# Kernel tuning notes

Hardware: AMD Instinct MI355X
Metric: run time of the kernel (lower is better)

## Reference

```python
import jax, jax.numpy as jnp
import numpy as np

B, S, D_IN, UNITS = 8, 2048, 512, 512


def _glorot(key, fan_in, fan_out):
    limit = np.sqrt(6.0 / (fan_in + fan_out)).astype(np.float32)
    return jax.random.uniform(key, (fan_in, fan_out), jnp.float32, -limit, limit)


def setup_inputs() -> dict:
    key = jax.random.key(0)
    kq, kwq, kwv, kwk = jax.random.split(key, 4)
    return {
        "query": jax.random.normal(kq, (B, S, D_IN), jnp.float32),
        "Wq": _glorot(kwq, D_IN, UNITS),   # W_query conv1d k=1, no bias
        "Wv": _glorot(kwv, D_IN, UNITS),   # W_value conv1d k=1, no bias
        "Wk": _glorot(kwk, D_IN, UNITS),   # W_key   conv1d k=1, no bias
    }


def reference(query, Wq, Wv, Wk):
    # Pointwise causal Conv1D(kernel=1, no bias) with sigmoid activation == sigmoid(x @ W)
    q = jax.nn.sigmoid(jnp.einsum('bsd,du->bsu', query, Wq))   # W_query(query)
    k = jax.nn.sigmoid(jnp.einsum('bsd,du->bsu', query, Wv))   # W_value(key=query)
    v = jax.nn.sigmoid(jnp.einsum('bsd,du->bsu', query, Wk))   # W_key(value=query)

    d_in = query.shape[-1]  # scaling uses value's input feature dim, not units
    score = jnp.einsum('bqu,bku->bqk', q, k) / jnp.sqrt(jnp.float32(d_in))  # [B,S,S]

    # Mask: upper triangle INCLUDING diagonal is -inf (strictly-causal, no self)
    s = score.shape[1]
    masked = jnp.where(jnp.triu(jnp.ones((s, s), bool)), -jnp.inf, score)

    # Row 0 is fully masked -> replaced by zeros; rows 1: softmax over j < i
    rest = jax.nn.softmax(masked[:, 1:, :], axis=-1)
    attn = jnp.concatenate([jnp.zeros((score.shape[0], 1, s), score.dtype), rest], axis=1)

    return jnp.einsum('bqk,bku->bqu', attn, v)
```

## Files before the change

### kernel.cpp

```cpp
#include <hip/hip_runtime.h>
#include <stdint.h>


typedef __attribute__((ext_vector_type(4))) float f32x4;
typedef __attribute__((ext_vector_type(8))) short short8;
typedef __attribute__((ext_vector_type(4))) short short4b;

__device__ __forceinline__ short f2bf(float f) {
    union { float f; uint32_t u; } v; v.f = f;
    uint32_t r = (v.u + 0x7FFFu + ((v.u >> 16) & 1u)) >> 16;
    return (short)r;
}
__device__ __forceinline__ float bf2f(short s) {
    union { uint32_t u; float f; } v; v.u = ((uint32_t)(uint16_t)s) << 16; return v.f;
}
__device__ __forceinline__ float sigm(float x) { return 1.0f / (1.0f + __expf(-x)); }

__device__ __forceinline__ void gload_lds16(const void* g, void* l) {
    __builtin_amdgcn_global_load_lds(
        (const __attribute__((address_space(1))) void*)g,
        (__attribute__((address_space(3))) void*)l, 16, 0, 0);
}

__global__ __launch_bounds__(256) void fused_prep(
    const float* __restrict__ X, const float* __restrict__ Wq,
    const float* __restrict__ Wv, const float* __restrict__ Wk,
    short* __restrict__ Xb, short* __restrict__ Wt)
{
    __shared__ float T[64 * 68];
    if (blockIdx.x < 4096) {
        size_t i = (size_t)blockIdx.x * 256 + threadIdx.x;
        const float4* src = reinterpret_cast<const float4*>(X) + i * 2;
        float4 a = src[0], b = src[1];
        short8 o;
        o[0] = f2bf(a.x); o[1] = f2bf(a.y); o[2] = f2bf(a.z); o[3] = f2bf(a.w);
        o[4] = f2bf(b.x); o[5] = f2bf(b.y); o[6] = f2bf(b.z); o[7] = f2bf(b.w);
        *reinterpret_cast<short8*>(Xb + i * 8) = o;
        return;
    }
    int bid = blockIdx.x - 4096;
    int w = bid >> 6;
    int tile = bid & 63;
    int n0 = (tile & 7) * 64;
    int k0 = (tile >> 3) * 64;
    const float* W = (w == 0) ? Wq : (w == 1) ? Wv : Wk;
    int t = threadIdx.x;
    int tr = t >> 4, tc = t & 15;
    for (int rr = 0; rr < 4; ++rr) {
        int row = rr * 16 + tr;
        float4 v = *reinterpret_cast<const float4*>(&W[(size_t)(k0 + row) * 512 + n0 + tc * 4]);
        T[row * 68 + tc * 4 + 0] = v.x;
        T[row * 68 + tc * 4 + 1] = v.y;
        T[row * 68 + tc * 4 + 2] = v.z;
        T[row * 68 + tc * 4 + 3] = v.w;
    }
    __syncthreads();
    for (int wr = 0; wr < 4; ++wr) {
        int nl = wr * 16 + tr;
        short4b o;
        for (int i = 0; i < 4; ++i) o[i] = f2bf(T[(tc * 4 + i) * 68 + nl]);
        *reinterpret_cast<short4b*>(&Wt[((size_t)(w * 512 + n0 + nl)) * 512 + k0 + tc * 4]) = o;
    }
}

__global__ __launch_bounds__(256) void qkv_gemm(
    const short* __restrict__ Xb,
    const short* __restrict__ Wt,
    short* __restrict__ Qb, short* __restrict__ Kb, short* __restrict__ VtG)
{
    __shared__ short SMEM[128 * 128];
    short* As = SMEM;
    short* Bs = SMEM + 128 * 64;

    int bx = blockIdx.x;
    int mt = bx & 127;
    int y = bx >> 7;
    int w = y >> 2, nt = y & 3;
    int m0 = mt * 128, n0 = nt * 128;

    int tid = threadIdx.x;
    int wv = tid >> 6, lane = tid & 63;
    int wr = wv >> 1, wc = wv & 1;
    int ln = lane & 15, hi = lane >> 4;

    f32x4 acc[4][4];
#pragma unroll
    for (int i = 0; i < 4; ++i)
#pragma unroll
        for (int j = 0; j < 4; ++j) acc[i][j] = {0.f, 0.f, 0.f, 0.f};

    const short* Asrc = Xb + (size_t)m0 * 512;
    const short* Bsrc = Wt + (size_t)w * 512 * 512 + (size_t)n0 * 512;

    for (int ko = 0; ko < 8; ++ko) {
        int k0 = ko * 64;
#pragma unroll
        for (int j = 0; j < 4; ++j) {
            int r = wv * 8 + j * 32 + (lane >> 3);
            int sc = ((lane & 7) * 8) ^ ((r & 7) << 3);
            gload_lds16(Asrc + (size_t)r * 512 + k0 + sc, &As[(wv * 8 + j * 32) * 64]);
        }
#pragma unroll
        for (int j = 0; j < 4; ++j) {
            int r = wv * 8 + j * 32 + (lane >> 3);
            int sc = ((lane & 7) * 8) ^ ((r & 7) << 3);
            gload_lds16(Bsrc + (size_t)r * 512 + k0 + sc, &Bs[(wv * 8 + j * 32) * 64]);
        }
        __syncthreads();
#pragma unroll
        for (int kk = 0; kk < 2; ++kk) {
            int kof = kk * 32 + hi * 8;
            int sw = (ln & 7) << 3;
            short8 af[4], bf[4];
#pragma unroll
            for (int mf = 0; mf < 4; ++mf)
                af[mf] = *reinterpret_cast<const short8*>(&As[(wr * 64 + mf * 16 + ln) * 64 + (kof ^ sw)]);
#pragma unroll
            for (int nf = 0; nf < 4; ++nf)
                bf[nf] = *reinterpret_cast<const short8*>(&Bs[(wc * 64 + nf * 16 + ln) * 64 + (kof ^ sw)]);
#pragma unroll
            for (int mf = 0; mf < 4; ++mf)
#pragma unroll
                for (int nf = 0; nf < 4; ++nf)
                    acc[mf][nf] = __builtin_amdgcn_mfma_f32_16x16x32_bf16(af[mf], bf[nf], acc[mf][nf], 0, 0, 0);
        }
        __syncthreads();
    }

    if (w < 2) {
        short* O = (w == 0) ? Qb : Kb;
#pragma unroll
        for (int mf = 0; mf < 4; ++mf)
#pragma unroll
            for (int nf = 0; nf < 4; ++nf)
#pragma unroll
                for (int j = 0; j < 4; ++j) {
                    int row = m0 + wr * 64 + mf * 16 + hi * 4 + j;
                    int col = n0 + wc * 64 + nf * 16 + ln;
                    O[(size_t)row * 512 + col] = f2bf(sigm(acc[mf][nf][j]));
                }
    } else {
#pragma unroll
        for (int mf = 0; mf < 4; ++mf)
#pragma unroll
            for (int nf = 0; nf < 4; ++nf)
#pragma unroll
                for (int j = 0; j < 4; ++j) {
                    int ml = wr * 64 + mf * 16 + hi * 4 + j;
                    int nl = wc * 64 + nf * 16 + ln;
                    SMEM[nl * 128 + (ml ^ ((nl & 7) << 3))] = f2bf(sigm(acc[mf][nf][j]));
                }
        __syncthreads();
        int bb = m0 >> 11;
        int s0 = m0 & 2047;
        int d = tid >> 1, h = tid & 1;
#pragma unroll
        for (int i = 0; i < 8; ++i) {
            int s8 = h * 64 + i * 8;
            short8 v = *reinterpret_cast<const short8*>(&SMEM[d * 128 + (s8 ^ ((d & 7) << 3))]);
            *reinterpret_cast<short8*>(&VtG[((size_t)(bb * 512 + n0 + d)) * 2048 + s0 + s8]) = v;
        }
    }
}

__global__ __launch_bounds__(256) void score_pass(
    const short* __restrict__ Qb, const short* __restrict__ Kb,
    short* __restrict__ Pc, float* __restrict__ Dpart)
{
    __shared__ short SMEM[128 * 128];
    __shared__ float psum[2][128];
    short* As = SMEM;
    short* Bs = SMEM + 128 * 64;

    const float scale = 0.044194173824159216f;

    int bid = blockIdx.x;
    int b = bid & 7;
    int idx = bid >> 3;
    int ti = 0;
    while ((ti + 1) * (ti + 2) / 2 <= idx) ++ti;
    int tj = idx - ti * (ti + 1) / 2;
    int m0 = ti * 128, n0 = tj * 128;

    int tid = threadIdx.x;
    int w = tid >> 6, lane = tid & 63;
    int wr = w >> 1, wc = w & 1;
    int ln = lane & 15, hi = lane >> 4;

    const short* Qsrc = Qb + (size_t)b * 2048 * 512 + (size_t)m0 * 512;
    const short* Ksrc = Kb + (size_t)b * 2048 * 512 + (size_t)n0 * 512;

    f32x4 acc[4][4];
#pragma unroll
    for (int i = 0; i < 4; ++i)
#pragma unroll
        for (int j = 0; j < 4; ++j) acc[i][j] = {0.f, 0.f, 0.f, 0.f};

    for (int ko = 0; ko < 8; ++ko) {
        int k0 = ko * 64;
#pragma unroll
        for (int j = 0; j < 4; ++j) {
            int r = w * 8 + j * 32 + (lane >> 3);
            int sc = ((lane & 7) * 8) ^ ((r & 7) << 3);
            gload_lds16(Qsrc + (size_t)r * 512 + k0 + sc, &As[(w * 8 + j * 32) * 64]);
        }
#pragma unroll
        for (int j = 0; j < 4; ++j) {
            int r = w * 8 + j * 32 + (lane >> 3);
            int sc = ((lane & 7) * 8) ^ ((r & 7) << 3);
            gload_lds16(Ksrc + (size_t)r * 512 + k0 + sc, &Bs[(w * 8 + j * 32) * 64]);
        }
        __syncthreads();
#pragma unroll
        for (int kk = 0; kk < 2; ++kk) {
            int kof = kk * 32 + hi * 8;
            int sw = (ln & 7) << 3;
            short8 af[4], bf[4];
#pragma unroll
            for (int mf = 0; mf < 4; ++mf)
                af[mf] = *reinterpret_cast<const short8*>(&As[(wr * 64 + mf * 16 + ln) * 64 + (kof ^ sw)]);
#pragma unroll
            for (int nf = 0; nf < 4; ++nf)
                bf[nf] = *reinterpret_cast<const short8*>(&Bs[(wc * 64 + nf * 16 + ln) * 64 + (kof ^ sw)]);
#pragma unroll
            for (int mf = 0; mf < 4; ++mf)
#pragma unroll
                for (int nf = 0; nf < 4; ++nf)
                    acc[mf][nf] = __builtin_amdgcn_mfma_f32_16x16x32_bf16(af[mf], bf[nf], acc[mf][nf], 0, 0, 0);
        }
        __syncthreads();
    }

    short* Ptile = Pc + (size_t)(b * 136 + idx) * 128 * 128;
#pragma unroll
    for (int mf = 0; mf < 4; ++mf) {
        float rs[4] = {0.f, 0.f, 0.f, 0.f};
#pragma unroll
        for (int nf = 0; nf < 4; ++nf)
#pragma unroll
            for (int j = 0; j < 4; ++j) {
                int rl = wr * 64 + mf * 16 + hi * 4 + j;
                int cl = wc * 64 + nf * 16 + ln;
                int irow = m0 + rl, jcol = n0 + cl;
                float p = (jcol < irow) ? __expf(acc[mf][nf][j] * scale) : 0.f;
                short hs = f2bf(p);
                Ptile[(size_t)rl * 128 + cl] = hs;
                rs[j] += bf2f(hs);
            }
#pragma unroll
        for (int j = 0; j < 4; ++j) {
            float s = rs[j];
            s += __shfl_xor(s, 1);
            s += __shfl_xor(s, 2);
            s += __shfl_xor(s, 4);
            s += __shfl_xor(s, 8);
            if (ln == 0) psum[wc][wr * 64 + mf * 16 + hi * 4 + j] = s;
        }
    }
    __syncthreads();
    if (tid < 128)
        Dpart[((size_t)b * 16 + tj) * 2048 + m0 + tid] = psum[0][tid] + psum[1][tid];
}

__global__ __launch_bounds__(256) void pv_pass(
    const short* __restrict__ Pc, const short* __restrict__ VtG,
    const float* __restrict__ Dpart, float* __restrict__ Out)
{
    __shared__ short SMEM[128 * 64 + 64 * 64];
    __shared__ float dnm[128];
    short* As = SMEM;
    short* Bs = SMEM + 128 * 64;

    int bid = blockIdx.x;
    int b = bid & 7;
    int rr = bid >> 3;
    int grp = rr >> 5, off = rr & 31;
    int ti = (grp & 1) ? (15 - (off >> 1)) : (off >> 1);
    int colhalf = 2 * grp + (off & 1);
    int m0 = ti * 128, n0 = colhalf * 64;

    int tid = threadIdx.x;
    int w = tid >> 6, lane = tid & 63;
    int wr = w >> 1, wc = w & 1;
    int ln = lane & 15, hi = lane >> 4;

    if (tid < 128) {
        float s = 0.f;
        for (int tj = 0; tj <= ti; ++tj)
            s += Dpart[((size_t)b * 16 + tj) * 2048 + m0 + tid];
        int gi = m0 + tid;
        dnm[tid] = (gi == 0) ? 0.f : 1.0f / s;
    }

    const short* Ptiles = Pc + (size_t)(b * 136 + ti * (ti + 1) / 2) * 128 * 128;
    const short* Vsrc = VtG + (size_t)b * 512 * 2048 + (size_t)n0 * 2048;

    f32x4 acc[4][2];
#pragma unroll
    for (int i = 0; i < 4; ++i)
#pragma unroll
        for (int j = 0; j < 2; ++j) acc[i][j] = {0.f, 0.f, 0.f, 0.f};

    for (int ks = 0; ks < 2 * (ti + 1); ++ks) {
        int tj = ks >> 1;
        int j0 = (ks & 1) * 64;
        const short* Pt = Ptiles + (size_t)tj * 128 * 128;
#pragma unroll
        for (int j = 0; j < 4; ++j) {
            int r = w * 8 + j * 32 + (lane >> 3);
            int sc = ((lane & 7) * 8) ^ ((r & 7) << 3);
            gload_lds16(Pt + (size_t)r * 128 + j0 + sc, &As[(w * 8 + j * 32) * 64]);
        }
#pragma unroll
        for (int j = 0; j < 2; ++j) {
            int r = w * 8 + j * 32 + (lane >> 3);
            int sc = ((lane & 7) * 8) ^ ((r & 7) << 3);
            gload_lds16(Vsrc + (size_t)r * 2048 + tj * 128 + j0 + sc, &Bs[(w * 8 + j * 32) * 64]);
        }
        __syncthreads();
#pragma unroll
        for (int kk = 0; kk < 2; ++kk) {
            int kof = kk * 32 + hi * 8;
            int sw = (ln & 7) << 3;
            short8 af[4], bf[2];
#pragma unroll
            for (int mf = 0; mf < 4; ++mf)
                af[mf] = *reinterpret_cast<const short8*>(&As[(wr * 64 + mf * 16 + ln) * 64 + (kof ^ sw)]);
#pragma unroll
            for (int nf = 0; nf < 2; ++nf)
                bf[nf] = *reinterpret_cast<const short8*>(&Bs[(wc * 32 + nf * 16 + ln) * 64 + (kof ^ sw)]);
#pragma unroll
            for (int mf = 0; mf < 4; ++mf)
#pragma unroll
                for (int nf = 0; nf < 2; ++nf)
                    acc[mf][nf] = __builtin_amdgcn_mfma_f32_16x16x32_bf16(af[mf], bf[nf], acc[mf][nf], 0, 0, 0);
        }
        __syncthreads();
    }

#pragma unroll
    for (int mf = 0; mf < 4; ++mf)
#pragma unroll
        for (int j = 0; j < 4; ++j) {
            int rl = wr * 64 + mf * 16 + hi * 4 + j;
            float rd = dnm[rl];
            float* orow = Out + ((size_t)b * 2048 + m0 + rl) * 512 + n0 + wc * 32 + ln;
#pragma unroll
            for (int nf = 0; nf < 2; ++nf)
                orow[nf * 16] = acc[mf][nf][j] * rd;
        }
}

extern "C" void kernel_launch(void* const* d_in, const int* in_sizes, int n_in,
                              void* d_out, int out_size, void* d_ws, size_t ws_size,
                              hipStream_t stream) {
    const float* X  = (const float*)d_in[0];
    const float* Wq = (const float*)d_in[1];
    const float* Wv = (const float*)d_in[2];
    const float* Wk = (const float*)d_in[3];
    float* Out = (float*)d_out;

    char* ws = (char*)d_ws;
    const size_t WT_BYTES  = (size_t)3 * 512 * 512 * 2;
    const size_t MAT_BYTES = (size_t)16384 * 512 * 2;
    const size_t PC_BYTES  = (size_t)8 * 136 * 128 * 128 * 2;
    short* Wt = (short*)ws;
    short* Qb = (short*)(ws + WT_BYTES);
    short* Kb = (short*)(ws + WT_BYTES + MAT_BYTES);
    short* Vt = (short*)(ws + WT_BYTES + 2 * MAT_BYTES);
    short* Pc = (short*)(ws + WT_BYTES + 3 * MAT_BYTES);
    short* Xb = Pc;
    float* Dp = (float*)(ws + WT_BYTES + 3 * MAT_BYTES + PC_BYTES);

    fused_prep<<<4288, 256, 0, stream>>>(X, Wq, Wv, Wk, Xb, Wt);
    qkv_gemm<<<1536, 256, 0, stream>>>(Xb, Wt, Qb, Kb, Vt);
    score_pass<<<1088, 256, 0, stream>>>(Qb, Kb, Pc, Dp);
    pv_pass<<<1024, 256, 0, stream>>>(Pc, Vt, Dp, Out);
}
```

Baseline: 136.4 us.

## Pair causal row tiles per PV block and load GEMM B fragments directly

pv_pass now runs 512-thread blocks that each process a complementary pair of causal row tiles (p and 15-p) over a 128-wide column slice, so every block gets the same amount of work. This also widens the N tile so each P tile load is shared by more output columns, and the launch shrinks to 256 blocks. Separately, qkv_gemm reads the weight fragments straight from global memory into registers instead of staging them through LDS. The trade-offs are fewer, heavier blocks (256 blocks on a GPU with many CUs), more accumulator registers, and uncoalesced-ish global B loads in the GEMM.

Result: slower. 158.8 us (+16.4%).

```diff
diff --git a/kernel.cpp b/kernel.cpp
--- a/kernel.cpp
+++ b/kernel.cpp
@@ -70,7 +70,6 @@
 {
     __shared__ short SMEM[128 * 128];
     short* As = SMEM;
-    short* Bs = SMEM + 128 * 64;
 
     int bx = blockIdx.x;
     int mt = bx & 127;
@@ -91,6 +90,7 @@
 
     const short* Asrc = Xb + (size_t)m0 * 512;
     const short* Bsrc = Wt + (size_t)w * 512 * 512 + (size_t)n0 * 512;
+    const short* Bfrag = Bsrc + (size_t)(wc * 64 + ln) * 512 + hi * 8;
 
     for (int ko = 0; ko < 8; ++ko) {
         int k0 = ko * 64;
@@ -100,29 +100,27 @@
             int sc = ((lane & 7) * 8) ^ ((r & 7) << 3);
             gload_lds16(Asrc + (size_t)r * 512 + k0 + sc, &As[(wv * 8 + j * 32) * 64]);
         }
-#pragma unroll
-        for (int j = 0; j < 4; ++j) {
-            int r = wv * 8 + j * 32 + (lane >> 3);
-            int sc = ((lane & 7) * 8) ^ ((r & 7) << 3);
-            gload_lds16(Bsrc + (size_t)r * 512 + k0 + sc, &Bs[(wv * 8 + j * 32) * 64]);
-        }
+        short8 breg[2][4];
+#pragma unroll
+        for (int kk = 0; kk < 2; ++kk)
+#pragma unroll
+            for (int nf = 0; nf < 4; ++nf)
+                breg[kk][nf] = *reinterpret_cast<const short8*>(
+                    Bfrag + (size_t)(nf * 16) * 512 + k0 + kk * 32);
         __syncthreads();
 #pragma unroll
         for (int kk = 0; kk < 2; ++kk) {
             int kof = kk * 32 + hi * 8;
             int sw = (ln & 7) << 3;
-            short8 af[4], bf[4];
+            short8 af[4];
 #pragma unroll
             for (int mf = 0; mf < 4; ++mf)
                 af[mf] = *reinterpret_cast<const short8*>(&As[(wr * 64 + mf * 16 + ln) * 64 + (kof ^ sw)]);
 #pragma unroll
-            for (int nf = 0; nf < 4; ++nf)
-                bf[nf] = *reinterpret_cast<const short8*>(&Bs[(wc * 64 + nf * 16 + ln) * 64 + (kof ^ sw)]);
-#pragma unroll
             for (int mf = 0; mf < 4; ++mf)
 #pragma unroll
                 for (int nf = 0; nf < 4; ++nf)
-                    acc[mf][nf] = __builtin_amdgcn_mfma_f32_16x16x32_bf16(af[mf], bf[nf], acc[mf][nf], 0, 0, 0);
+                    acc[mf][nf] = __builtin_amdgcn_mfma_f32_16x16x32_bf16(af[mf], breg[kk][nf], acc[mf][nf], 0, 0, 0);
         }
         __syncthreads();
     }
@@ -262,93 +260,105 @@
         Dpart[((size_t)b * 16 + tj) * 2048 + m0 + tid] = psum[0][tid] + psum[1][tid];
 }
 
-__global__ __launch_bounds__(256) void pv_pass(
+__global__ __launch_bounds__(512) void pv_pass(
     const short* __restrict__ Pc, const short* __restrict__ VtG,
     const float* __restrict__ Dpart, float* __restrict__ Out)
 {
-    __shared__ short SMEM[128 * 64 + 64 * 64];
-    __shared__ float dnm[128];
-    short* As = SMEM;
-    short* Bs = SMEM + 128 * 64;
+    __shared__ short As[128 * 64];
+    __shared__ short Bs[128 * 64];
+    __shared__ float dnm[2][128];
 
     int bid = blockIdx.x;
     int b = bid & 7;
-    int rr = bid >> 3;
-    int grp = rr >> 5, off = rr & 31;
-    int ti = (grp & 1) ? (15 - (off >> 1)) : (off >> 1);
-    int colhalf = 2 * grp + (off & 1);
-    int m0 = ti * 128, n0 = colhalf * 64;
+    int r5 = bid >> 3;
+    int p = r5 & 7;
+    int dq = r5 >> 3;
+    int n0 = dq * 128;
 
     int tid = threadIdx.x;
-    int w = tid >> 6, lane = tid & 63;
-    int wr = w >> 1, wc = w & 1;
+    int wv = tid >> 6, lane = tid & 63;
+    int wm = wv >> 2, wn = wv & 3;
     int ln = lane & 15, hi = lane >> 4;
 
-    if (tid < 128) {
+    if (tid < 256) {
+        int g = tid >> 7, row = tid & 127;
+        int ti = g ? (15 - p) : p;
         float s = 0.f;
         for (int tj = 0; tj <= ti; ++tj)
-            s += Dpart[((size_t)b * 16 + tj) * 2048 + m0 + tid];
-        int gi = m0 + tid;
-        dnm[tid] = (gi == 0) ? 0.f : 1.0f / s;
-    }
-
-    const short* Ptiles = Pc + (size_t)(b * 136 + ti * (ti + 1) / 2) * 128 * 128;
+            s += Dpart[((size_t)b * 16 + tj) * 2048 + ti * 128 + row];
+        int gi = ti * 128 + row;
+        dnm[g][row] = (gi == 0) ? 0.f : 1.0f / s;
+    }
+
     const short* Vsrc = VtG + (size_t)b * 512 * 2048 + (size_t)n0 * 2048;
 
-    f32x4 acc[4][2];
-#pragma unroll
-    for (int i = 0; i < 4; ++i)
-#pragma unroll
-        for (int j = 0; j < 2; ++j) acc[i][j] = {0.f, 0.f, 0.f, 0.f};
-
-    for (int ks = 0; ks < 2 * (ti + 1); ++ks) {
-        int tj = ks >> 1;
-        int j0 = (ks & 1) * 64;
-        const short* Pt = Ptiles + (size_t)tj * 128 * 128;
-#pragma unroll
-        for (int j = 0; j < 4; ++j) {
-            int r = w * 8 + j * 32 + (lane >> 3);
-            int sc = ((lane & 7) * 8) ^ ((r & 7) << 3);
-            gload_lds16(Pt + (size_t)r * 128 + j0 + sc, &As[(w * 8 + j * 32) * 64]);
-        }
-#pragma unroll
-        for (int j = 0; j < 2; ++j) {
-            int r = w * 8 + j * 32 + (lane >> 3);
-            int sc = ((lane & 7) * 8) ^ ((r & 7) << 3);
-            gload_lds16(Vsrc + (size_t)r * 2048 + tj * 128 + j0 + sc, &Bs[(w * 8 + j * 32) * 64]);
-        }
-        __syncthreads();
-#pragma unroll
-        for (int kk = 0; kk < 2; ++kk) {
-            int kof = kk * 32 + hi * 8;
-            int sw = (ln & 7) << 3;
-            short8 af[4], bf[2];
-#pragma unroll
-            for (int mf = 0; mf < 4; ++mf)
-                af[mf] = *reinterpret_cast<const short8*>(&As[(wr * 64 + mf * 16 + ln) * 64 + (kof ^ sw)]);
-#pragma unroll
-            for (int nf = 0; nf < 2; ++nf)
-                bf[nf] = *reinterpret_cast<const short8*>(&Bs[(wc * 32 + nf * 16 + ln) * 64 + (kof ^ sw)]);
-#pragma unroll
-            for (int mf = 0; mf < 4; ++mf)
+    f32x4 acc[2][4][2];
+#pragma unroll
+    for (int g = 0; g < 2; ++g)
+#pragma unroll
+        for (int i = 0; i < 4; ++i)
+#pragma unroll
+            for (int j = 0; j < 2; ++j) acc[g][i][j] = {0.f, 0.f, 0.f, 0.f};
+
+#pragma unroll
+    for (int g = 0; g < 2; ++g) {
+        int ti = g ? (15 - p) : p;
+        const short* Ptiles = Pc + (size_t)(b * 136 + ti * (ti + 1) / 2) * 16384;
+        for (int ks = 0; ks < 2 * (ti + 1); ++ks) {
+            int tj = ks >> 1;
+            int j0 = (ks & 1) * 64;
+            const short* Pt = Ptiles + (size_t)tj * 16384;
+#pragma unroll
+            for (int j = 0; j < 2; ++j) {
+                int r0 = wv * 16 + j * 8;
+                int r = r0 + (lane >> 3);
+                int sc = ((lane & 7) * 8) ^ ((r & 7) << 3);
+                gload_lds16(Pt + (size_t)r * 128 + j0 + sc, &As[r0 * 64]);
+            }
+#pragma unroll
+            for (int j = 0; j < 2; ++j) {
+                int r0 = wv * 16 + j * 8;
+                int r = r0 + (lane >> 3);
+                int sc = ((lane & 7) * 8) ^ ((r & 7) << 3);
+                gload_lds16(Vsrc + (size_t)r * 2048 + tj * 128 + j0 + sc, &Bs[r0 * 64]);
+            }
+            __syncthreads();
+#pragma unroll
+            for (int kk = 0; kk < 2; ++kk) {
+                int kof = kk * 32 + hi * 8;
+                int sw = (ln & 7) << 3;
+                short8 af[4], bf[2];
+#pragma unroll
+                for (int mf = 0; mf < 4; ++mf)
+                    af[mf] = *reinterpret_cast<const short8*>(&As[(wm * 64 + mf * 16 + ln) * 64 + (kof ^ sw)]);
 #pragma unroll
                 for (int nf = 0; nf < 2; ++nf)
-                    acc[mf][nf] = __builtin_amdgcn_mfma_f32_16x16x32_bf16(af[mf], bf[nf], acc[mf][nf], 0, 0, 0);
-        }
-        __syncthreads();
-    }
-
-#pragma unroll
-    for (int mf = 0; mf < 4; ++mf)
-#pragma unroll
-        for (int j = 0; j < 4; ++j) {
-            int rl = wr * 64 + mf * 16 + hi * 4 + j;
-            float rd = dnm[rl];
-            float* orow = Out + ((size_t)b * 2048 + m0 + rl) * 512 + n0 + wc * 32 + ln;
-#pragma unroll
-            for (int nf = 0; nf < 2; ++nf)
-                orow[nf * 16] = acc[mf][nf][j] * rd;
-        }
+                    bf[nf] = *reinterpret_cast<const short8*>(&Bs[(wn * 32 + nf * 16 + ln) * 64 + (kof ^ sw)]);
+#pragma unroll
+                for (int mf = 0; mf < 4; ++mf)
+#pragma unroll
+                    for (int nf = 0; nf < 2; ++nf)
+                        acc[g][mf][nf] = __builtin_amdgcn_mfma_f32_16x16x32_bf16(af[mf], bf[nf], acc[g][mf][nf], 0, 0, 0);
+            }
+            __syncthreads();
+        }
+    }
+
+#pragma unroll
+    for (int g = 0; g < 2; ++g) {
+        int ti = g ? (15 - p) : p;
+#pragma unroll
+        for (int mf = 0; mf < 4; ++mf)
+#pragma unroll
+            for (int j = 0; j < 4; ++j) {
+                int rl = wm * 64 + mf * 16 + hi * 4 + j;
+                float rd = dnm[g][rl];
+                float* orow = Out + ((size_t)b * 2048 + ti * 128 + rl) * 512 + n0 + wn * 32 + ln;
+#pragma unroll
+                for (int nf = 0; nf < 2; ++nf)
+                    orow[nf * 16] = acc[g][mf][nf][j] * rd;
+            }
+    }
 }
 
 extern "C" void kernel_launch(void* const* d_in, const int* in_sizes, int n_in,
@@ -375,5 +385,5 @@
     fused_prep<<<4288, 256, 0, stream>>>(X, Wq, Wv, Wk, Xb, Wt);
     qkv_gemm<<<1536, 256, 0, stream>>>(Xb, Wt, Qb, Kb, Vt);
     score_pass<<<1088, 256, 0, stream>>>(Qb, Kb, Pc, Dp);
-    pv_pass<<<1024, 256, 0, stream>>>(Pc, Vt, Dp, Out);
-}
+    pv_pass<<<256, 512, 0, stream>>>(Pc, Vt, Dp, Out);
+}
```

## Double-buffer QKV GEMM LDS loads and stage Q/K epilogue through LDS

Applied to the files above, without the earlier changes.

The QKV projection GEMM now keeps two LDS buffers and issues the global-to-LDS loads for the next K step before computing on the current one, using one waitcnt+barrier per iteration instead of two syncthreads. The Q/K epilogue now writes sigmoid outputs into a swizzled LDS tile and stores them with 16-byte vector writes, replacing scattered 2-byte global stores. Launch bounds hint two blocks per CU. LDS use doubles to 64 KB per block, which can limit occupancy. The qkv GEMM is only one of several kernels, so the effect on total time is bounded.

After: 132.7 us, median of 2. -2.7%, faster.

```diff
diff --git a/kernel.cpp b/kernel.cpp
--- a/kernel.cpp
+++ b/kernel.cpp
@@ -21,6 +21,8 @@
         (const __attribute__((address_space(1))) void*)g,
         (__attribute__((address_space(3))) void*)l, 16, 0, 0);
 }
+
+#define VMBAR() asm volatile("s_waitcnt vmcnt(0)\n\ts_barrier" ::: "memory")
 
 __global__ __launch_bounds__(256) void fused_prep(
     const float* __restrict__ X, const float* __restrict__ Wq,
@@ -63,14 +65,12 @@
     }
 }
 
-__global__ __launch_bounds__(256) void qkv_gemm(
+__global__ __launch_bounds__(256, 2) void qkv_gemm(
     const short* __restrict__ Xb,
     const short* __restrict__ Wt,
     short* __restrict__ Qb, short* __restrict__ Kb, short* __restrict__ VtG)
 {
-    __shared__ short SMEM[128 * 128];
-    short* As = SMEM;
-    short* Bs = SMEM + 128 * 64;
+    __shared__ short SMEM[2][16384];
 
     int bx = blockIdx.x;
     int mt = bx & 127;
@@ -92,21 +92,34 @@
     const short* Asrc = Xb + (size_t)m0 * 512;
     const short* Bsrc = Wt + (size_t)w * 512 * 512 + (size_t)n0 * 512;
 
+    int srow = wv * 8 + (lane >> 3);
+    int ssc0 = (lane & 7) * 8;
+
+#define QSTAGE(ko, buf)                                                            \
+    {                                                                              \
+        int _k0 = (ko) * 64;                                                       \
+        _Pragma("unroll")                                                          \
+        for (int _j = 0; _j < 4; ++_j) {                                           \
+            int _r = srow + _j * 32;                                               \
+            int _sc = ssc0 ^ ((_r & 7) << 3);                                      \
+            gload_lds16(Asrc + (size_t)_r * 512 + _k0 + _sc,                       \
+                        &SMEM[buf][(wv * 8 + _j * 32) * 64]);                      \
+        }                                                                          \
+        _Pragma("unroll")                                                          \
+        for (int _j = 0; _j < 4; ++_j) {                                           \
+            int _r = srow + _j * 32;                                               \
+            int _sc = ssc0 ^ ((_r & 7) << 3);                                      \
+            gload_lds16(Bsrc + (size_t)_r * 512 + _k0 + _sc,                       \
+                        &SMEM[buf][8192 + (wv * 8 + _j * 32) * 64]);               \
+        }                                                                          \
+    }
+
+    QSTAGE(0, 0);
     for (int ko = 0; ko < 8; ++ko) {
-        int k0 = ko * 64;
-#pragma unroll
-        for (int j = 0; j < 4; ++j) {
-            int r = wv * 8 + j * 32 + (lane >> 3);
-            int sc = ((lane & 7) * 8) ^ ((r & 7) << 3);
-            gload_lds16(Asrc + (size_t)r * 512 + k0 + sc, &As[(wv * 8 + j * 32) * 64]);
-        }
-#pragma unroll
-        for (int j = 0; j < 4; ++j) {
-            int r = wv * 8 + j * 32 + (lane >> 3);
-            int sc = ((lane & 7) * 8) ^ ((r & 7) << 3);
-            gload_lds16(Bsrc + (size_t)r * 512 + k0 + sc, &Bs[(wv * 8 + j * 32) * 64]);
-        }
-        __syncthreads();
+        VMBAR();
+        if (ko + 1 < 8) QSTAGE(ko + 1, (ko + 1) & 1);
+        const short* As = SMEM[ko & 1];
+        const short* Bs = SMEM[ko & 1] + 8192;
 #pragma unroll
         for (int kk = 0; kk < 2; ++kk) {
             int kof = kk * 32 + hi * 8;
@@ -124,21 +137,31 @@
                 for (int nf = 0; nf < 4; ++nf)
                     acc[mf][nf] = __builtin_amdgcn_mfma_f32_16x16x32_bf16(af[mf], bf[nf], acc[mf][nf], 0, 0, 0);
         }
-        __syncthreads();
-    }
-
+    }
+    __syncthreads();
+#undef QSTAGE
+
+    short* Ts = SMEM[0];
     if (w < 2) {
+#pragma unroll
+        for (int mf = 0; mf < 4; ++mf)
+#pragma unroll
+            for (int nf = 0; nf < 4; ++nf)
+#pragma unroll
+                for (int j = 0; j < 4; ++j) {
+                    int rl = wr * 64 + mf * 16 + hi * 4 + j;
+                    int cl = wc * 64 + nf * 16 + ln;
+                    Ts[rl * 128 + (cl ^ ((rl & 7) << 3))] = f2bf(sigm(acc[mf][nf][j]));
+                }
+        __syncthreads();
         short* O = (w == 0) ? Qb : Kb;
-#pragma unroll
-        for (int mf = 0; mf < 4; ++mf)
-#pragma unroll
-            for (int nf = 0; nf < 4; ++nf)
-#pragma unroll
-                for (int j = 0; j < 4; ++j) {
-                    int row = m0 + wr * 64 + mf * 16 + hi * 4 + j;
-                    int col = n0 + wc * 64 + nf * 16 + ln;
-                    O[(size_t)row * 512 + col] = f2bf(sigm(acc[mf][nf][j]));
-                }
+        int r = tid >> 1, h = tid & 1;
+#pragma unroll
+        for (int i = 0; i < 8; ++i) {
+            int c8 = h * 64 + i * 8;
+            short8 v = *reinterpret_cast<const short8*>(&Ts[r * 128 + (c8 ^ ((r & 7) << 3))]);
+            *reinterpret_cast<short8*>(&O[(size_t)(m0 + r) * 512 + n0 + c8]) = v;
+        }
     } else {
 #pragma unroll
         for (int mf = 0; mf < 4; ++mf)
@@ -148,7 +171,7 @@
                 for (int j = 0; j < 4; ++j) {
                     int ml = wr * 64 + mf * 16 + hi * 4 + j;
                     int nl = wc * 64 + nf * 16 + ln;
-                    SMEM[nl * 128 + (ml ^ ((nl & 7) << 3))] = f2bf(sigm(acc[mf][nf][j]));
+                    Ts[nl * 128 + (ml ^ ((nl & 7) << 3))] = f2bf(sigm(acc[mf][nf][j]));
                 }
         __syncthreads();
         int bb = m0 >> 11;
@@ -157,7 +180,7 @@
 #pragma unroll
         for (int i = 0; i < 8; ++i) {
             int s8 = h * 64 + i * 8;
-            short8 v = *reinterpret_cast<const short8*>(&SMEM[d * 128 + (s8 ^ ((d & 7) << 3))]);
+            short8 v = *reinterpret_cast<const short8*>(&Ts[d * 128 + (s8 ^ ((d & 7) << 3))]);
             *reinterpret_cast<short8*>(&VtG[((size_t)(bb * 512 + n0 + d)) * 2048 + s0 + s8]) = v;
         }
     }
```
